# Kernel optimization log

Hardware: AMD Instinct MI355X
Metric: run time of the kernel (lower is better)

The kernel has to match this reference:

```python
import jax, jax.numpy as jnp
import numpy as np

EPS = 1e-5

@jax.custom_vjp
def spike(u):
    return (u >= 0).astype(u.dtype)

def _spike_fwd(u):
    return spike(u), u

def _spike_bwd(u, g):
    return (g / (1.0 + 5.0 * jnp.abs(u)) ** 2,)

spike.defvjp(_spike_fwd, _spike_bwd)


def setup_inputs() -> dict:
    key = jax.random.key(0)
    ks = jax.random.split(key, 20)
    B, T, IN, TH, H = 2048, 320, 64, 128, 64
    d = {}
    d['x'] = jax.random.normal(ks[0], (B, T, IN), jnp.float32)
    d['tda'] = jax.random.normal(ks[1], (B, 150), jnp.float32)
    # depthwise conv: Conv1d(64,128,k=15,pad=7,groups=64) -> kernel [128, 1, 15]
    d['conv_w'] = jax.random.normal(ks[2], (TH, 1, 15), jnp.float32) * 0.1
    d['conv_b'] = jnp.zeros((TH,), jnp.float32)
    d['bn1_g'] = jnp.ones((TH,), jnp.float32)
    d['bn1_b'] = jnp.zeros((TH,), jnp.float32)
    d['bn1_m'] = jnp.zeros((TH,), jnp.float32)
    d['bn1_v'] = jnp.ones((TH,), jnp.float32)
    # spatial_fc: Linear(128,64), init mean=0.05 std=0.1
    d['sp_w'] = 0.05 + 0.1 * jax.random.normal(ks[3], (H, TH), jnp.float32)
    d['sp_b'] = jnp.zeros((H,), jnp.float32)
    d['li_w'] = jax.random.normal(ks[4], (H, 2 * H), jnp.float32) * (1.0 / np.sqrt(2 * H))
    d['li_b'] = jnp.zeros((H,), jnp.float32)
    d['tda_w1'] = jax.random.normal(ks[5], (64, 150), jnp.float32) * (1.0 / np.sqrt(150))
    d['tda_b1'] = jnp.zeros((64,), jnp.float32)
    d['tda_w2'] = jax.random.normal(ks[6], (32, 64), jnp.float32) * 0.125
    d['tda_b2'] = jnp.zeros((32,), jnp.float32)
    dp_out = (320 // 32) * H  # 640
    d['cls_w1'] = jax.random.normal(ks[7], (128, dp_out + 32), jnp.float32) * (1.0 / np.sqrt(dp_out + 32))
    d['cls_b1'] = jnp.zeros((128,), jnp.float32)
    d['bn2_g'] = jnp.ones((128,), jnp.float32)
    d['bn2_b'] = jnp.zeros((128,), jnp.float32)
    d['bn2_m'] = jnp.zeros((128,), jnp.float32)
    d['bn2_v'] = jnp.ones((128,), jnp.float32)
    d['cls_w2'] = jax.random.normal(ks[8], (4, 128), jnp.float32) * (1.0 / np.sqrt(128))
    d['cls_b2'] = jnp.zeros((4,), jnp.float32)
    return d


def reference(x, tda, conv_w, conv_b, bn1_g, bn1_b, bn1_m, bn1_v, sp_w, sp_b,
              li_w, li_b, tda_w1, tda_b1, tda_w2, tda_b2,
              cls_w1, cls_b1, bn2_g, bn2_b, bn2_m, bn2_v, cls_w2, cls_b2):
    B, T, _ = x.shape
    L_DP, N_DP, H = 32, 16, 64
    # temp_conv (eval mode: no dropout, BN with running stats)
    xc = jnp.transpose(x, (0, 2, 1))  # [B, 64, T]
    y = jax.lax.conv_general_dilated(
        xc, conv_w, window_strides=(1,), padding=[(7, 7)],
        dimension_numbers=('NCH', 'OIH', 'NCH'), feature_group_count=64)
    y = y + conv_b[None, :, None]
    y = (y - bn1_m[None, :, None]) * jax.lax.rsqrt(bn1_v + EPS)[None, :, None] * bn1_g[None, :, None] + bn1_b[None, :, None]
    y = jax.nn.relu(y)
    y = jnp.transpose(y, (0, 2, 1))  # [B, T, 128]
    # precompute all input currents: [T, B, 64] (time-major for scan)
    cur_all = jnp.einsum('bth,oh->tbo', y, sp_w) + sp_b

    def step(carry, cur):
        mf, ms, ml = carry
        mf = 0.5 * mf + cur
        sf = spike(mf - 0.5)
        mf = mf * (1.0 - sf)
        ms = 0.9 * ms + cur
        ss = spike(ms - 1.0)
        ms = ms * (1.0 - ss)
        cur_li = jnp.concatenate([sf, ss], axis=-1) @ li_w.T + li_b
        ml = 0.9 * ml + cur_li
        return (mf, ms, ml), ml

    z0 = jnp.zeros((B, H), x.dtype)
    _, li_seq = jax.lax.scan(step, (z0, z0, z0), cur_all)  # [T, B, 64]
    li_seq = jnp.transpose(li_seq, (1, 0, 2))  # [B, T, 64]

    windows = li_seq.reshape(B, T // L_DP, L_DP, H)
    start_mean = windows[:, :, :N_DP, :].mean(axis=2)
    end_mean = windows[:, :, -N_DP:, :].mean(axis=2)
    dp_feat = (end_mean - start_mean).reshape(B, -1)  # [B, 640]

    t1 = jax.nn.relu(tda @ tda_w1.T + tda_b1)
    tda_feat = jax.nn.relu(t1 @ tda_w2.T + tda_b2)  # [B, 32]

    h = jnp.concatenate([dp_feat, tda_feat], axis=-1) @ cls_w1.T + cls_b1
    h = (h - bn2_m) * jax.lax.rsqrt(bn2_v + EPS) * bn2_g + bn2_b
    h = jax.nn.relu(h)
    return h @ cls_w2.T + cls_b2  # [B, 4]
```

## Files before the change

### kernel.cpp

```cpp
#include <hip/hip_runtime.h>

#define NT 256

#define WS_SPWT    0
#define WS_SC1     8192
#define WS_SH1     8320
#define WS_SC2     8448
#define WS_SH2     8576
#define WS_LIWT    8704
#define WS_TW1T    16896
#define WS_TW2T    26496
#define WS_CW1T    28544
#define WS_TOTAL   114560
#define WS_WG      114560
#define WS_WBASE   114688

__global__ void prep_kernel(
    const float* __restrict__ conv_b, const float* __restrict__ bn1_g,
    const float* __restrict__ bn1_b,  const float* __restrict__ bn1_m,
    const float* __restrict__ bn1_v,  const float* __restrict__ sp_w,
    const float* __restrict__ li_w,   const float* __restrict__ tda_w1,
    const float* __restrict__ tda_w2, const float* __restrict__ cls_w1,
    const float* __restrict__ bn2_g,  const float* __restrict__ bn2_b,
    const float* __restrict__ bn2_m,  const float* __restrict__ bn2_v,
    float* __restrict__ ws)
{
    int i = blockIdx.x * NT + threadIdx.x;
    if (i > WS_TOTAL) return;
    if (i == WS_TOTAL) {
        float g = 0.f, sE = 0.f, sL = 0.f; int w = 0;
        for (int t = 0; t < 320; ++t) {
            g = fmaf(0.9f, g, 1.f);
            int pos = t & 31;
            if (pos < 16) sE += g; else sL += g;
            if (pos == 31) { ws[WS_WG + w] = sL - sE; ++w; sE = 0.f; sL = 0.f; }
        }
        return;
    }
    if (i < WS_SC1) {
        int c = i >> 6, h = i & 63;
        ws[i] = sp_w[h*128 + c];
    } else if (i < WS_SH1) {
        int c = i - WS_SC1;
        float vv = bn1_v[c] + 1e-5f;
        ws[i] = (float)((double)bn1_g[c] / sqrt((double)vv));
    } else if (i < WS_SC2) {
        int c = i - WS_SH1;
        float vv = bn1_v[c] + 1e-5f;
        double s = (double)bn1_g[c] / sqrt((double)vv);
        ws[i] = (float)(((double)conv_b[c] - (double)bn1_m[c])*s + (double)bn1_b[c]);
    } else if (i < WS_SH2) {
        int c = i - WS_SC2;
        float vv = bn2_v[c] + 1e-5f;
        ws[i] = (float)((double)bn2_g[c] / sqrt((double)vv));
    } else if (i < WS_LIWT) {
        int c = i - WS_SH2;
        float vv = bn2_v[c] + 1e-5f;
        double s = (double)bn2_g[c] / sqrt((double)vv);
        ws[i] = (float)((double)bn2_b[c] - (double)bn2_m[c]*s);
    } else if (i < WS_TW1T) {
        int t = i - WS_LIWT; int j = t >> 6, o = t & 63;
        ws[i] = li_w[o*128 + j];
    } else if (i < WS_TW2T) {
        int t = i - WS_TW1T; int r = t >> 6, o = t & 63;
        ws[i] = tda_w1[o*150 + r];
    } else if (i < WS_CW1T) {
        int t = i - WS_TW2T; int j = t >> 5, o = t & 31;
        ws[i] = tda_w2[o*64 + j];
    } else {
        int t = i - WS_CW1T; int j = t >> 7, c = t & 127;
        ws[i] = cls_w1[c*672 + j];
    }
}

__launch_bounds__(NT, 3)
__global__ void fused_kernel(
    const float* __restrict__ x, const float* __restrict__ conv_w,
    const float* __restrict__ sp_b, const float* __restrict__ ws,
    float* __restrict__ wfeat)
{
    __shared__ float y_lds[128*65];
    __shared__ float cur_lds[64*64];

    const int tid  = threadIdx.x;
    const int b    = blockIdx.x;
    const int ic   = tid & 63;
    const int tg   = tid >> 6;
    const int lane = tid & 63;
    const int wid  = tid >> 6;
    const int h0   = __builtin_amdgcn_readfirstlane((tid >> 6) << 4);
    const int sw   = (int)(((unsigned)b * 2654435761u) >> 30);

    float w0[15], w1[15];
    #pragma unroll
    for (int k = 0; k < 15; ++k) {
        w0[k] = conv_w[(2*ic)*15 + k];
        w1[k] = conv_w[(2*ic + 1)*15 + k];
    }
    const float sA = ws[WS_SC1 + 2*ic],     hA = ws[WS_SH1 + 2*ic];
    const float sB = ws[WS_SC1 + 2*ic + 1], hB = ws[WS_SH1 + 2*ic + 1];
    const float4* bp = reinterpret_cast<const float4*>(sp_b + h0);
    const float4 b0v = bp[0], b1v = bp[1], b2v = bp[2], b3v = bp[3];

    const float* __restrict__ spwT = ws;
    const float* xb = x + (size_t)b * 20480 + ic;
    float* Wb = wfeat + (size_t)b * 1280;

    float mf = 0.f, ms = 0.f, rlo = 0.f, rhi = 0.f;

    float xr0[30], xr1[30];
    #pragma unroll
    for (int r = 0; r < 30; ++r) {
        int t = tg*16 - 7 + r;
        xr0[r] = (t >= 0) ? xb[(size_t)t * 64] : 0.f;
    }
    #pragma unroll
    for (int j = 0; j < 16; ++j) {
        float a0 = 0.f, a1 = 0.f;
        #pragma unroll
        for (int k = 0; k < 15; ++k) {
            a0 = fmaf(xr0[j + k], w0[k], a0);
            a1 = fmaf(xr0[j + k], w1[k], a1);
        }
        int tt = tg*16 + j;
        y_lds[(2*ic)*65 + tt]     = fmaxf(fmaf(a0, sA, hA), 0.f);
        y_lds[(2*ic + 1)*65 + tt] = fmaxf(fmaf(a1, sB, hB), 0.f);
    }
    __syncthreads();

    #pragma unroll
    for (int chk = 0; chk < 5; ++chk) {
        float* xn = (chk & 1) ? xr0 : xr1;

        if (chk < 4) {
            const int tbase = (chk + 1)*64 + tg*16 - 7;
            if (tbase + 29 < 320) {
                #pragma unroll
                for (int r = 0; r < 30; ++r)
                    xn[r] = xb[(size_t)(tbase + r) * 64];
            } else {
                #pragma unroll
                for (int r = 0; r < 30; ++r) {
                    int t = tbase + r;
                    xn[r] = (t < 320) ? xb[(size_t)t * 64] : 0.f;
                }
            }
        }

        {
            float acc[16];
            acc[0]=b0v.x;  acc[1]=b0v.y;  acc[2]=b0v.z;  acc[3]=b0v.w;
            acc[4]=b1v.x;  acc[5]=b1v.y;  acc[6]=b1v.z;  acc[7]=b1v.w;
            acc[8]=b2v.x;  acc[9]=b2v.y;  acc[10]=b2v.z; acc[11]=b2v.w;
            acc[12]=b3v.x; acc[13]=b3v.y; acc[14]=b3v.z; acc[15]=b3v.w;

            #pragma unroll 4
            for (int c = 0; c < 128; ++c) {
                float yv = y_lds[c*65 + lane];
                const float4* wp = reinterpret_cast<const float4*>(spwT + c*64 + h0);
                float4 q0 = wp[0], q1 = wp[1], q2 = wp[2], q3 = wp[3];
                acc[0]  = fmaf(yv, q0.x, acc[0]);
                acc[1]  = fmaf(yv, q0.y, acc[1]);
                acc[2]  = fmaf(yv, q0.z, acc[2]);
                acc[3]  = fmaf(yv, q0.w, acc[3]);
                acc[4]  = fmaf(yv, q1.x, acc[4]);
                acc[5]  = fmaf(yv, q1.y, acc[5]);
                acc[6]  = fmaf(yv, q1.z, acc[6]);
                acc[7]  = fmaf(yv, q1.w, acc[7]);
                acc[8]  = fmaf(yv, q2.x, acc[8]);
                acc[9]  = fmaf(yv, q2.y, acc[9]);
                acc[10] = fmaf(yv, q2.z, acc[10]);
                acc[11] = fmaf(yv, q2.w, acc[11]);
                acc[12] = fmaf(yv, q3.x, acc[12]);
                acc[13] = fmaf(yv, q3.y, acc[13]);
                acc[14] = fmaf(yv, q3.z, acc[14]);
                acc[15] = fmaf(yv, q3.w, acc[15]);
            }
            const int tsw = (lane & 15) << 2;
            #pragma unroll
            for (int k = 0; k < 4; ++k) {
                float4 v4 = make_float4(acc[4*k], acc[4*k+1], acc[4*k+2], acc[4*k+3]);
                *reinterpret_cast<float4*>(&cur_lds[lane*64 + ((h0 + 4*k) ^ tsw)]) = v4;
            }
        }
        __syncthreads();

        if (wid == sw) {
            float sE_lo = 0.f, sE_hi = 0.f;
            #pragma unroll
            for (int gq = 0; gq < 4; ++gq) {
                float v[16];
                #pragma unroll
                for (int q = 0; q < 16; ++q) {
                    int t = gq*16 + q;
                    v[q] = cur_lds[t*64 + (lane ^ ((t & 15) << 2))];
                }
                float slo = 0.f, shi = 0.f;
                #pragma unroll
                for (int q = 0; q < 16; ++q) {
                    float c = v[q];
                    mf = fmaf(0.5f, mf, c);
                    bool sf = mf >= 0.5f;
                    ms = fmaf(0.9f, ms, c);
                    bool ss = ms >= 1.0f;
                    mf = sf ? 0.f : mf;
                    ms = ss ? 0.f : ms;
                    rlo = fmaf(0.9f, rlo, sf ? 1.f : 0.f);
                    rhi = fmaf(0.9f, rhi, ss ? 1.f : 0.f);
                    slo += rlo; shi += rhi;
                }
                if ((gq & 1) == 0) {
                    sE_lo = slo; sE_hi = shi;
                } else {
                    int wdx = chk*2 + (gq >> 1);
                    Wb[wdx*128 + lane]      = slo - sE_lo;
                    Wb[wdx*128 + 64 + lane] = shi - sE_hi;
                }
            }
        }
        if (chk < 4) {
            #pragma unroll
            for (int j = 0; j < 16; ++j) {
                float a0 = 0.f, a1 = 0.f;
                #pragma unroll
                for (int k = 0; k < 15; ++k) {
                    a0 = fmaf(xn[j + k], w0[k], a0);
                    a1 = fmaf(xn[j + k], w1[k], a1);
                }
                int tt = tg*16 + j;
                y_lds[(2*ic)*65 + tt]     = fmaxf(fmaf(a0, sA, hA), 0.f);
                y_lds[(2*ic + 1)*65 + tt] = fmaxf(fmaf(a1, sB, hB), 0.f);
            }
        }
        __syncthreads();
    }
}

__global__ void epilogue_kernel(
    const float* __restrict__ tda,    const float* __restrict__ li_b,
    const float* __restrict__ tda_b1, const float* __restrict__ tda_b2,
    const float* __restrict__ cls_b1, const float* __restrict__ cls_w2,
    const float* __restrict__ cls_b2, const float* __restrict__ ws,
    const float* __restrict__ W,      float* __restrict__ out)
{
    __shared__ float Wl[1280];
    __shared__ float t1[64], tf[32], dp[640], h1[128];
    const int b = blockIdx.x, tid = threadIdx.x;

    for (int i = tid; i < 1280; i += NT)
        Wl[i] = W[(size_t)b*1280 + i];
    __syncthreads();

    const float* __restrict__ liwT = ws + WS_LIWT;
    const float* __restrict__ tw1T = ws + WS_TW1T;
    const float* __restrict__ tw2T = ws + WS_TW2T;
    const float* __restrict__ cw1T = ws + WS_CW1T;
    const float* tdab = tda + b*150;

    if (tid < 64) {
        float acc = tda_b1[tid];
        for (int i2 = 0; i2 < 150; ++i2)
            acc = fmaf(tdab[i2], tw1T[i2*64 + tid], acc);
        t1[tid] = fmaxf(acc, 0.f);
    }
    __syncthreads();
    if (tid < 32) {
        float acc = tda_b2[tid];
        #pragma unroll 8
        for (int j = 0; j < 64; ++j)
            acc = fmaf(t1[j], tw2T[j*32 + tid], acc);
        tf[tid] = fmaxf(acc, 0.f);
    }
    {
        int o = tid & 63;
        for (int w = tid >> 6; w < 10; w += 4) {
            float acc = li_b[o] * ws[WS_WG + w];
            #pragma unroll 4
            for (int j = 0; j < 128; ++j)
                acc = fmaf(Wl[w*128 + j], liwT[j*64 + o], acc);
            dp[w*64 + o] = 0.0625f * acc;
        }
    }
    __syncthreads();
    if (tid < 128) {
        float acc = cls_b1[tid];
        for (int j = 0; j < 640; ++j)
            acc = fmaf(dp[j], cw1T[j*128 + tid], acc);
        #pragma unroll 4
        for (int j = 0; j < 32; ++j)
            acc = fmaf(tf[j], cw1T[(640 + j)*128 + tid], acc);
        float s2 = ws[WS_SC2 + tid], sh2 = ws[WS_SH2 + tid];
        h1[tid] = fmaxf(fmaf(acc, s2, sh2), 0.f);
    }
    __syncthreads();
    if (tid < 4) {
        float acc = cls_b2[tid];
        for (int c = 0; c < 128; ++c)
            acc = fmaf(h1[c], cls_w2[tid*128 + c], acc);
        out[b*4 + tid] = acc;
    }
}

extern "C" void kernel_launch(void* const* d_in, const int* in_sizes, int n_in,
                              void* d_out, int out_size, void* d_ws, size_t ws_size,
                              hipStream_t stream) {
    const float* x      = (const float*)d_in[0];
    const float* tda    = (const float*)d_in[1];
    const float* conv_w = (const float*)d_in[2];
    const float* conv_b = (const float*)d_in[3];
    const float* bn1_g  = (const float*)d_in[4];
    const float* bn1_b  = (const float*)d_in[5];
    const float* bn1_m  = (const float*)d_in[6];
    const float* bn1_v  = (const float*)d_in[7];
    const float* sp_w   = (const float*)d_in[8];
    const float* sp_b   = (const float*)d_in[9];
    const float* li_w   = (const float*)d_in[10];
    const float* li_b   = (const float*)d_in[11];
    const float* tda_w1 = (const float*)d_in[12];
    const float* tda_b1 = (const float*)d_in[13];
    const float* tda_w2 = (const float*)d_in[14];
    const float* tda_b2 = (const float*)d_in[15];
    const float* cls_w1 = (const float*)d_in[16];
    const float* cls_b1 = (const float*)d_in[17];
    const float* bn2_g  = (const float*)d_in[18];
    const float* bn2_b  = (const float*)d_in[19];
    const float* bn2_m  = (const float*)d_in[20];
    const float* bn2_v  = (const float*)d_in[21];
    const float* cls_w2 = (const float*)d_in[22];
    const float* cls_b2 = (const float*)d_in[23];
    float* ws  = (float*)d_ws;
    float* out = (float*)d_out;

    const int B = in_sizes[0] / (320 * 64);

    prep_kernel<<<(WS_TOTAL + 1 + NT - 1)/NT, NT, 0, stream>>>(
        conv_b, bn1_g, bn1_b, bn1_m, bn1_v, sp_w,
        li_w, tda_w1, tda_w2, cls_w1,
        bn2_g, bn2_b, bn2_m, bn2_v, ws);

    fused_kernel<<<B, NT, 0, stream>>>(
        x, conv_w, sp_b, ws, ws + WS_WBASE);

    epilogue_kernel<<<B, NT, 0, stream>>>(
        tda, li_b, tda_b1, tda_b2, cls_b1, cls_w2, cls_b2,
        ws, ws + WS_WBASE, out);
}
```

Baseline: 256.5 us.

## Compute spatial FC on MFMA with split bf16 hi/lo operands

Replaces the scalar FP32 FMA loop for the 128->64 spatial projection with MFMA 16x16x32 bf16 instructions. Both weights and activations are split into high and low bf16 parts, and four MFMAs per k-step keep accuracy close to fp32. Activations are stored in LDS as swizzled bf16 hi/lo planes, and the spiking wave is fixed to wave 0. This moves the matmul off the VALU onto the matrix cores, at the cost of extra conversion work, a 4x MFMA count, and slightly reduced precision.

```diff
diff --git a/kernel.cpp b/kernel.cpp
--- a/kernel.cpp
+++ b/kernel.cpp
@@ -2,7 +2,18 @@
 
 #define NT 256
 
-#define WS_SPWT    0
+typedef __attribute__((ext_vector_type(8))) short short8b;
+typedef __attribute__((ext_vector_type(4))) float f32x4;
+
+__device__ inline unsigned short f2bf(float f) {
+    unsigned u = __float_as_uint(f);
+    unsigned r = (u + 0x7fffu + ((u >> 16) & 1u)) >> 16;
+    return (unsigned short)r;
+}
+__device__ inline float bf2f(unsigned short h) {
+    return __uint_as_float(((unsigned)h) << 16);
+}
+
 #define WS_SC1     8192
 #define WS_SH1     8320
 #define WS_SC2     8448
@@ -37,9 +48,12 @@
         }
         return;
     }
-    if (i < WS_SC1) {
-        int c = i >> 6, h = i & 63;
-        ws[i] = sp_w[h*128 + c];
+    if (i < 8192) {
+        unsigned short* ws16 = (unsigned short*)ws;
+        float v = sp_w[i];
+        unsigned short hv = f2bf(v);
+        ws16[i] = hv;
+        ws16[8192 + i] = f2bf(v - bf2f(hv));
     } else if (i < WS_SH1) {
         int c = i - WS_SC1;
         float vv = bn1_v[c] + 1e-5f;
@@ -79,7 +93,7 @@
     const float* __restrict__ sp_b, const float* __restrict__ ws,
     float* __restrict__ wfeat)
 {
-    __shared__ float y_lds[128*65];
+    __shared__ unsigned short ylds[2][64*128];
     __shared__ float cur_lds[64*64];
 
     const int tid  = threadIdx.x;
@@ -88,8 +102,9 @@
     const int tg   = tid >> 6;
     const int lane = tid & 63;
     const int wid  = tid >> 6;
-    const int h0   = __builtin_amdgcn_readfirstlane((tid >> 6) << 4);
-    const int sw   = (int)(((unsigned)b * 2654435761u) >> 30);
+    const int kg   = lane >> 4;
+    const int ha   = lane & 15;
+    const int tl   = tg*16 + ha;
 
     float w0[15], w1[15];
     #pragma unroll
@@ -99,10 +114,13 @@
     }
     const float sA = ws[WS_SC1 + 2*ic],     hA = ws[WS_SH1 + 2*ic];
     const float sB = ws[WS_SC1 + 2*ic + 1], hB = ws[WS_SH1 + 2*ic + 1];
-    const float4* bp = reinterpret_cast<const float4*>(sp_b + h0);
-    const float4 b0v = bp[0], b1v = bp[1], b2v = bp[2], b3v = bp[3];
-
-    const float* __restrict__ spwT = ws;
+    f32x4 spb4[4];
+    #pragma unroll
+    for (int mt = 0; mt < 4; ++mt)
+        spb4[mt] = *reinterpret_cast<const f32x4*>(sp_b + mt*16 + kg*4);
+
+    const unsigned short* wsh = (const unsigned short*)ws;
+    const unsigned short* wsl = wsh + 8192;
     const float* xb = x + (size_t)b * 20480 + ic;
     float* Wb = wfeat + (size_t)b * 1280;
 
@@ -122,9 +140,14 @@
             a0 = fmaf(xr0[j + k], w0[k], a0);
             a1 = fmaf(xr0[j + k], w1[k], a1);
         }
+        float y0 = fmaxf(fmaf(a0, sA, hA), 0.f);
+        float y1 = fmaxf(fmaf(a1, sB, hB), 0.f);
         int tt = tg*16 + j;
-        y_lds[(2*ic)*65 + tt]     = fmaxf(fmaf(a0, sA, hA), 0.f);
-        y_lds[(2*ic + 1)*65 + tt] = fmaxf(fmaf(a1, sB, hB), 0.f);
+        unsigned off = (unsigned)(tt*256) + (((unsigned)(ic*4)) ^ ((unsigned)((tt & 7) << 4)));
+        unsigned short y0h = f2bf(y0), y1h = f2bf(y1);
+        unsigned short y0l = f2bf(y0 - bf2f(y0h)), y1l = f2bf(y1 - bf2f(y1h));
+        *(unsigned*)((char*)&ylds[0][0] + off) = (unsigned)y0h | ((unsigned)y1h << 16);
+        *(unsigned*)((char*)&ylds[1][0] + off) = (unsigned)y0l | ((unsigned)y1l << 16);
     }
     __syncthreads();
 
@@ -148,44 +171,36 @@
         }
 
         {
-            float acc[16];
-            acc[0]=b0v.x;  acc[1]=b0v.y;  acc[2]=b0v.z;  acc[3]=b0v.w;
-            acc[4]=b1v.x;  acc[5]=b1v.y;  acc[6]=b1v.z;  acc[7]=b1v.w;
-            acc[8]=b2v.x;  acc[9]=b2v.y;  acc[10]=b2v.z; acc[11]=b2v.w;
-            acc[12]=b3v.x; acc[13]=b3v.y; acc[14]=b3v.z; acc[15]=b3v.w;
-
-            #pragma unroll 4
-            for (int c = 0; c < 128; ++c) {
-                float yv = y_lds[c*65 + lane];
-                const float4* wp = reinterpret_cast<const float4*>(spwT + c*64 + h0);
-                float4 q0 = wp[0], q1 = wp[1], q2 = wp[2], q3 = wp[3];
-                acc[0]  = fmaf(yv, q0.x, acc[0]);
-                acc[1]  = fmaf(yv, q0.y, acc[1]);
-                acc[2]  = fmaf(yv, q0.z, acc[2]);
-                acc[3]  = fmaf(yv, q0.w, acc[3]);
-                acc[4]  = fmaf(yv, q1.x, acc[4]);
-                acc[5]  = fmaf(yv, q1.y, acc[5]);
-                acc[6]  = fmaf(yv, q1.z, acc[6]);
-                acc[7]  = fmaf(yv, q1.w, acc[7]);
-                acc[8]  = fmaf(yv, q2.x, acc[8]);
-                acc[9]  = fmaf(yv, q2.y, acc[9]);
-                acc[10] = fmaf(yv, q2.z, acc[10]);
-                acc[11] = fmaf(yv, q2.w, acc[11]);
-                acc[12] = fmaf(yv, q3.x, acc[12]);
-                acc[13] = fmaf(yv, q3.y, acc[13]);
-                acc[14] = fmaf(yv, q3.z, acc[14]);
-                acc[15] = fmaf(yv, q3.w, acc[15]);
-            }
-            const int tsw = (lane & 15) << 2;
+            short8b Bh[4], Bl[4];
+            const unsigned tswz = (unsigned)((tl & 7) << 4);
             #pragma unroll
-            for (int k = 0; k < 4; ++k) {
-                float4 v4 = make_float4(acc[4*k], acc[4*k+1], acc[4*k+2], acc[4*k+3]);
-                *reinterpret_cast<float4*>(&cur_lds[lane*64 + ((h0 + 4*k) ^ tsw)]) = v4;
+            for (int ks = 0; ks < 4; ++ks) {
+                unsigned off = (unsigned)(tl*256) + (((unsigned)(ks*64 + kg*16)) ^ tswz);
+                Bh[ks] = *(const short8b*)((const char*)&ylds[0][0] + off);
+                Bl[ks] = *(const short8b*)((const char*)&ylds[1][0] + off);
+            }
+            #pragma unroll
+            for (int mt = 0; mt < 4; ++mt) {
+                const unsigned short* ap = wsh + (mt*16 + ha)*128;
+                const unsigned short* lp = wsl + (mt*16 + ha)*128;
+                f32x4 acc = spb4[mt];
+                #pragma unroll
+                for (int ks = 0; ks < 4; ++ks) {
+                    short8b Ah = *(const short8b*)(ap + ks*32 + kg*8);
+                    short8b Al = *(const short8b*)(lp + ks*32 + kg*8);
+                    acc = __builtin_amdgcn_mfma_f32_16x16x32_bf16(Ah, Bh[ks], acc, 0, 0, 0);
+                    acc = __builtin_amdgcn_mfma_f32_16x16x32_bf16(Ah, Bl[ks], acc, 0, 0, 0);
+                    acc = __builtin_amdgcn_mfma_f32_16x16x32_bf16(Al, Bh[ks], acc, 0, 0, 0);
+                    acc = __builtin_amdgcn_mfma_f32_16x16x32_bf16(Al, Bl[ks], acc, 0, 0, 0);
+                }
+                const int hb = mt*16 + kg*4;
+                *reinterpret_cast<f32x4*>(
+                    &cur_lds[tl*64 + (hb ^ ((tl & 15) << 2))]) = acc;
             }
         }
         __syncthreads();
 
-        if (wid == sw) {
+        if (wid == 0) {
             float sE_lo = 0.f, sE_hi = 0.f;
             #pragma unroll
             for (int gq = 0; gq < 4; ++gq) {
@@ -227,9 +242,14 @@
                     a0 = fmaf(xn[j + k], w0[k], a0);
                     a1 = fmaf(xn[j + k], w1[k], a1);
                 }
+                float y0 = fmaxf(fmaf(a0, sA, hA), 0.f);
+                float y1 = fmaxf(fmaf(a1, sB, hB), 0.f);
                 int tt = tg*16 + j;
-                y_lds[(2*ic)*65 + tt]     = fmaxf(fmaf(a0, sA, hA), 0.f);
-                y_lds[(2*ic + 1)*65 + tt] = fmaxf(fmaf(a1, sB, hB), 0.f);
+                unsigned off = (unsigned)(tt*256) + (((unsigned)(ic*4)) ^ ((unsigned)((tt & 7) << 4)));
+                unsigned short y0h = f2bf(y0), y1h = f2bf(y1);
+                unsigned short y0l = f2bf(y0 - bf2f(y0h)), y1l = f2bf(y1 - bf2f(y1h));
+                *(unsigned*)((char*)&ylds[0][0] + off) = (unsigned)y0h | ((unsigned)y1h << 16);
+                *(unsigned*)((char*)&ylds[1][0] + off) = (unsigned)y0l | ((unsigned)y1l << 16);
             }
         }
         __syncthreads();
```

Measured after the change: 295.5 us. +15.2%, slower.
